# Performance work log

Measured on AMD Instinct MI355X. Metric: run time of the kernel, lower is better.

## Reference

```python
import jax, jax.numpy as jnp
import numpy as np

BN_EPS = 1e-5

def _bn(x, gamma, beta):
    # BatchNorm1d in training mode: batch mean, biased variance
    m = jnp.mean(x, axis=0)
    v = jnp.var(x, axis=0)
    return (x - m) * jax.lax.rsqrt(v + BN_EPS) * gamma + beta

def setup_inputs() -> dict:
    key = jax.random.key(0)
    ks = jax.random.split(key, 12)
    N, E, D, ED = 50000, 600000, 128, 16
    s = lambda k, sh: jax.random.normal(k, sh, dtype=jnp.float32) * 0.05
    return {
        'h': jax.random.normal(ks[0], (N, D), dtype=jnp.float32),
        'edge_index': jax.random.randint(ks[1], (2, E), 0, N, dtype=jnp.int64),
        'edge_attr': jax.random.normal(ks[2], (E, ED), dtype=jnp.float32),
        'ee_w1': s(ks[3], (ED, D)), 'ee_b1': jnp.zeros((D,), jnp.float32),
        'ee_g1': jnp.ones((D,), jnp.float32), 'ee_bb1': jnp.zeros((D,), jnp.float32),
        'ee_w2': s(ks[4], (D, D)), 'ee_b2': jnp.zeros((D,), jnp.float32),
        'mlp_w1': s(ks[5], (D, D)), 'mlp_b1': jnp.zeros((D,), jnp.float32),
        'mlp_g1': jnp.ones((D,), jnp.float32), 'mlp_bb1': jnp.zeros((D,), jnp.float32),
        'mlp_w2': s(ks[6], (D, D)), 'mlp_b2': jnp.zeros((D,), jnp.float32),
        'mlp_g2': jnp.ones((D,), jnp.float32), 'mlp_bb2': jnp.zeros((D,), jnp.float32),
    }

def reference(h, edge_index, edge_attr, ee_w1, ee_b1, ee_g1, ee_bb1, ee_w2, ee_b2,
              mlp_w1, mlp_b1, mlp_g1, mlp_bb1, mlp_w2, mlp_b2, mlp_g2, mlp_bb2):
    N = h.shape[0]
    src, dst = edge_index[0], edge_index[1]
    # edge_encoder: Linear -> BN -> ReLU -> Linear
    e = jax.nn.relu(_bn(edge_attr @ ee_w1 + ee_b1, ee_g1, ee_bb1)) @ ee_w2 + ee_b2  # [E, D]
    # scatter-add edge embeddings to destination nodes
    agg_edge = jax.ops.segment_sum(e, dst, num_segments=N)  # [N, D]
    h = h + agg_edge
    # GINConv (eps=0): mlp(h + sum_{j->i} h_j)
    neigh = jax.ops.segment_sum(h[src], dst, num_segments=N)  # [N, D]
    z = h + neigh
    z = jax.nn.relu(_bn(z @ mlp_w1 + mlp_b1, mlp_g1, mlp_bb1))
    z = jax.nn.relu(_bn(z @ mlp_w2 + mlp_b2, mlp_g2, mlp_bb2))
    return z
```

## Files before the change

kernel.cpp:

```cpp
#include <hip/hip_runtime.h>
#include <hip/hip_bf16.h>

#define DD 128
#define EDIM 16
#define WPB 4
#define PSE 68
#define NCOPY 16

typedef short v8s __attribute__((ext_vector_type(8)));
typedef float v4f __attribute__((ext_vector_type(4)));

__device__ __forceinline__ float ldf(const void* p, int i, int bf){
  return bf ? __bfloat162float(((const __hip_bfloat16*)p)[i])
            : ((const float*)p)[i];
}
__device__ __forceinline__ float bfu_lo(unsigned u){
  unsigned b = (u & 0xffffu) << 16; float f; __builtin_memcpy(&f,&b,4); return f;
}
__device__ __forceinline__ float bfu_hi(unsigned u){
  unsigned b = u & 0xffff0000u; float f; __builtin_memcpy(&f,&b,4); return f;
}
__device__ __forceinline__ unsigned short f2bf(float f){
  unsigned u; __builtin_memcpy(&u,&f,4);
  unsigned r = (u + 0x7fffu + ((u>>16)&1u)) >> 16;
  return (unsigned short)r;
}
__device__ __forceinline__ unsigned packbf(float a, float b){
  return (unsigned)f2bf(a) | ((unsigned)f2bf(b) << 16);
}

__global__ void k_detect(const void* g1, const int* ei, int E, int* flags){
  __shared__ int nz;
  if (threadIdx.x==0) nz = 0;
  __syncthreads();
  long long total = 2LL*E;
  long long stride = (total/1024) & ~1LL;
  if (stride < 2) stride = 2;
  long long idx = (long long)threadIdx.x*stride + 1;
  if (idx < total && ei[idx] != 0) atomicAdd(&nz, 1);
  __syncthreads();
  if (threadIdx.x==0){
    unsigned w = *(const unsigned*)g1;
    flags[0] = (w == 0x3F803F80u) ? 1 : 0;
    flags[1] = (nz == 0) ? 1 : 0;
  }
}

__global__ void k_transB(const void* w0, const void* w1, const void* w2,
                         const void* we1, const int* __restrict__ flags,
                         short* __restrict__ Bt){
  const int bf = flags[0];
  for (int idx = blockIdx.x*blockDim.x + threadIdx.x; idx < 3*16384 + 2048;
       idx += gridDim.x*blockDim.x){
    if (idx < 3*16384){
      int m = idx >> 14, r = idx & 16383;
      int nn = r >> 7, k = r & 127;
      const void* w = (m==0) ? w0 : ((m==1) ? w1 : w2);
      Bt[idx] = (short)f2bf(ldf(w, k*DD + nn, bf));
    } else {
      int r = idx - 3*16384;
      int nn = r >> 4, k = r & 15;
      Bt[idx] = (short)f2bf(ldf(we1, k*DD + nn, bf));
    }
  }
}

__global__ __launch_bounds__(256) void k_attr_moments(
    const void* __restrict__ attr, int E, const int* __restrict__ flags,
    float* __restrict__ Ssum , float* __restrict__ csum )
{
  __shared__ short Ws[4*512];
  __shared__ float sred[4][256];
  __shared__ float credu[4][16];
  const int t = threadIdx.x;
  const int wv = t >> 6, lane = t & 63, l15 = lane & 15, quad = lane >> 4;
  const int bf = flags[0];
  const int el = lane >> 1, half = lane & 1;
  short* W = &Ws[wv*512];

  v4f acc = (v4f){0.f,0.f,0.f,0.f};
  float cs[8];
  #pragma unroll
  for (int j=0;j<8;++j) cs[j]=0.f;

  const int nchunks = (E + 31) >> 5;
  for (int c = blockIdx.x*4 + wv; c < nchunks; c += gridDim.x*4){
    const int e = c*32 + el;
    const bool ok = (e < E);
    float f[8];
    if (bf){
      uint4 u = {0u,0u,0u,0u};
      if (ok) u = reinterpret_cast<const uint4*>(attr)[(size_t)e*2 + half];
      f[0]=bfu_lo(u.x); f[1]=bfu_hi(u.x); f[2]=bfu_lo(u.y); f[3]=bfu_hi(u.y);
      f[4]=bfu_lo(u.z); f[5]=bfu_hi(u.z); f[6]=bfu_lo(u.w); f[7]=bfu_hi(u.w);
    } else {
      float4 v0 = {0,0,0,0}, v1 = {0,0,0,0};
      if (ok){
        const float4* ap = reinterpret_cast<const float4*>(attr) +
                           (size_t)e*4 + half*2;
        v0 = ap[0]; v1 = ap[1];
      }
      f[0]=v0.x; f[1]=v0.y; f[2]=v0.z; f[3]=v0.w;
      f[4]=v1.x; f[5]=v1.y; f[6]=v1.z; f[7]=v1.w;
    }
    #pragma unroll
    for (int j=0;j<8;++j){
      cs[j] += f[j];
      W[(half*8 + j)*32 + el] = (short)f2bf(f[j]);
    }
    v8s a = *reinterpret_cast<const v8s*>(&W[l15*32 + quad*8]);
    acc = __builtin_amdgcn_mfma_f32_16x16x32_bf16(a, a, acc, 0,0,0);
  }

  #pragma unroll
  for (int r=0;r<4;++r) sred[wv][(quad*4 + r)*16 + l15] = acc[r];
  #pragma unroll
  for (int j=0;j<8;++j){
    #pragma unroll
    for (int off=2; off<64; off<<=1) cs[j] += __shfl_xor(cs[j], off, 64);
  }
  if (lane < 2){
    #pragma unroll
    for (int j=0;j<8;++j) credu[wv][lane*8 + j] = cs[j];
  }
  __syncthreads();
  const int cp = blockIdx.x & (NCOPY-1);
  float s = sred[0][t]+sred[1][t]+sred[2][t]+sred[3][t];
  atomicAdd(&Ssum[cp*256 + t], s);
  if (t < 16){
    float s2 = credu[0][t]+credu[1][t]+credu[2][t]+credu[3][t];
    atomicAdd(&csum[cp*16 + t], s2);
  }
}

__global__ void k_edge_bn(const void* __restrict__ w1, const void* __restrict__ g,
                          const void* __restrict__ bb,
                          const float* __restrict__ Ssum, const float* __restrict__ csum,
                          float Einv, const int* __restrict__ flags,
                          float* __restrict__ sc, float* __restrict__ sh){
  __shared__ float fS[256];
  __shared__ float fc[16];
  const int j = threadIdx.x;
  const int bf = flags[0];
  {
    float a0 = 0.f, a1 = 0.f;
    #pragma unroll
    for (int c=0;c<NCOPY;++c){ a0 += Ssum[c*256 + j]; a1 += Ssum[c*256 + 128 + j]; }
    fS[j] = a0; fS[128+j] = a1;
    if (j < 16){
      float a2 = 0.f;
      #pragma unroll
      for (int c=0;c<NCOPY;++c) a2 += csum[c*16 + j];
      fc[j] = a2;
    }
  }
  __syncthreads();
  float w[EDIM];
  #pragma unroll
  for (int p=0;p<EDIM;++p) w[p] = ldf(w1, p*DD + j, bf);
  float mu0 = 0.f;
  #pragma unroll
  for (int p=0;p<EDIM;++p) mu0 += fc[p]*Einv*w[p];
  float s2 = 0.f;
  #pragma unroll
  for (int p=0;p<EDIM;++p){
    float acc = 0.f;
    #pragma unroll
    for (int q=0;q<EDIM;++q) acc += fS[p*16 + q]*w[q];
    s2 += w[p]*acc;
  }
  float var = s2*Einv - mu0*mu0;
  float scv = ldf(g, j, bf) * rsqrtf(var + 1e-5f);
  sc[j] = scv;
  sh[j] = ldf(bb, j, bf) - mu0*scv;
}

__global__ void k_hist(const int* __restrict__ ei, int E,
                       const int* __restrict__ flags, int* __restrict__ deg){
  const int i64 = flags[1];
  const int2* ei2 = (const int2*)ei;
  for (int e = blockIdx.x*blockDim.x + threadIdx.x; e < E;
       e += gridDim.x*blockDim.x){
    int d = i64 ? ei2[E + e].x : ei[E + e];
    atomicAdd(&deg[d], 1);
  }
}

__global__ void k_scan_partial(const int* __restrict__ deg, int n,
                               int* __restrict__ bsum){
  __shared__ int red[256];
  const int t = threadIdx.x;
  const int base = blockIdx.x*1024;
  int s = 0;
  for (int i = t; i < 1024; i += 256){
    int g = base + i;
    s += (g < n) ? deg[g] : 0;
  }
  red[t] = s; __syncthreads();
  for (int off=128; off>0; off>>=1){
    if (t < off) red[t] += red[t+off];
    __syncthreads();
  }
  if (t==0) bsum[blockIdx.x] = red[0];
}

__global__ void k_scan_tops(int* __restrict__ bsum, int nb, int* __restrict__ total){
  __shared__ int buf[256];
  const int t = threadIdx.x;
  int v = (t < nb) ? bsum[t] : 0;
  buf[t] = v; __syncthreads();
  for (int off=1; off<256; off<<=1){
    int x = (t>=off) ? buf[t-off] : 0;
    __syncthreads();
    buf[t] += x; __syncthreads();
  }
  if (t < nb) bsum[t] = buf[t] - v;
  if (t == 255) *total = buf[255];
}

__global__ void k_scan_final(const int* __restrict__ deg, int n, int nwin,
                             const int* __restrict__ bsum, const int* __restrict__ total,
                             int* __restrict__ offsets, int* __restrict__ cursor,
                             int* __restrict__ win2node){
  __shared__ int red[256];
  const int t = threadIdx.x;
  const int base = blockIdx.x*1024 + t*4;
  int v[4]; int s = 0;
  #pragma unroll
  for (int k=0;k<4;++k){
    int g = base + k;
    v[k] = (g < n) ? deg[g] : 0;
    s += v[k];
  }
  red[t] = s; __syncthreads();
  for (int off=1; off<256; off<<=1){
    int x = (t>=off) ? red[t-off] : 0;
    __syncthreads();
    red[t] += x; __syncthreads();
  }
  int ex = bsum[blockIdx.x] + red[t] - s;
  #pragma unroll
  for (int k=0;k<4;++k){
    int g = base + k;
    if (g < n){
      offsets[g] = ex; cursor[g] = ex;
      int end = ex + v[k];
      for (int w = (ex + 63) >> 6; (w << 6) < end; ++w) win2node[w] = g;
    }
    ex += v[k];
  }
  if (blockIdx.x==0 && t==0){
    offsets[n] = *total;
    win2node[nwin] = n - 1;
  }
}

__global__ void k_scatter(const int* __restrict__ ei, int E,
                          const int* __restrict__ flags,
                          int* __restrict__ cursor, int2* __restrict__ se){
  const int i64 = flags[1];
  const int2* ei2 = (const int2*)ei;
  for (int e = blockIdx.x*blockDim.x + threadIdx.x; e < E;
       e += gridDim.x*blockDim.x){
    int d = i64 ? ei2[E + e].x : ei[E + e];
    int s = i64 ? ei2[e].x     : ei[e];
    int pp = atomicAdd(&cursor[d], 1);
    se[pp] = make_int2(s, e);
  }
}

__global__ __launch_bounds__(256) void k_edgeagg(
    const void* __restrict__ attr, const int2* __restrict__ se,
    const short* __restrict__ w1t,
    const float* __restrict__ sc, const float* __restrict__ sh,
    const int* __restrict__ offsets, const int* __restrict__ win2node,
    const int* __restrict__ flags, int n, int E, float* __restrict__ Pagg)
{
  __shared__ __align__(16) float Ps[DD*PSE];
  const int t = threadIdx.x;
  const int wv = t >> 6, lane = t & 63, l15 = lane & 15, quad = lane >> 4;
  const int bf = flags[0];
  const int G0 = blockIdx.x * (64*WPB);
  if (G0 >= E) return;

  const int4 w2nv = *reinterpret_cast<const int4*>(&win2node[blockIdx.x*WPB]);
  const int w2na[4] = {w2nv.x, w2nv.y, w2nv.z, w2nv.w};
  const int w2next = win2node[blockIdx.x*WPB + WPB];

  v8s afrag[WPB];
  #pragma unroll
  for (int w=0; w<WPB; ++w){
    afrag[w] = (v8s){0,0,0,0,0,0,0,0};
    if (quad < 2){
      int slot = G0 + w*64 + wv*16 + l15;
      if (slot < E){
        int e = se[slot].y;
        if (bf){
          afrag[w] = *reinterpret_cast<const v8s*>(
                (const short*)attr + (size_t)e*EDIM + quad*8);
        } else {
          const float4* ap = reinterpret_cast<const float4*>(
                (const float*)attr + (size_t)e*EDIM + quad*8);
          float4 v0 = ap[0], v1 = ap[1];
          v8s av;
          av[0]=(short)f2bf(v0.x); av[1]=(short)f2bf(v0.y);
          av[2]=(short)f2bf(v0.z); av[3]=(short)f2bf(v0.w);
          av[4]=(short)f2bf(v1.x); av[5]=(short)f2bf(v1.y);
          av[6]=(short)f2bf(v1.z); av[7]=(short)f2bf(v1.w);
          afrag[w] = av;
        }
      }
    }
  }

  v8s bfrag[8];
  #pragma unroll
  for (int cg=0;cg<8;++cg){
    bfrag[cg] = (v8s){0,0,0,0,0,0,0,0};
    if (quad < 2)
      bfrag[cg] = *reinterpret_cast<const v8s*>(&w1t[(cg*16+l15)*EDIM + quad*8]);
  }
  const float scA = sc[lane],      shA = sh[lane];
  const float scB = sc[lane + 64], shB = sh[lane + 64];

  #pragma unroll
  for (int w=0; w<WPB; ++w){
    const int B0 = G0 + w*64;
    if (B0 >= E) break;
    const int Bend = (B0 + 64 < E) ? (B0 + 64) : E;

    #pragma unroll
    for (int cg=0;cg<8;++cg){
      v4f acc = (v4f){0.f,0.f,0.f,0.f};
      acc = __builtin_amdgcn_mfma_f32_16x16x32_bf16(bfrag[cg], afrag[w], acc, 0,0,0);
      #pragma unroll
      for (int reg=0;reg<4;++reg)
        Ps[(cg*16 + quad*4 + reg)*PSE + wv*16 + l15] = acc[reg];
    }
    __syncthreads();

    const int i1 = (w < WPB-1) ? w2na[w+1] : w2next;
    int idx = w2na[w] + wv;
    int nb = 0, ne = 0;
    if (idx <= i1){ nb = offsets[idx]; ne = offsets[idx+1]; }
    while (idx <= i1){
      const int idxn = idx + 4;
      int nbn = 0, nen = 0;
      if (idxn <= i1){ nbn = offsets[idxn]; nen = offsets[idxn+1]; }
      int s0 = nb - B0; if (s0 < 0) s0 = 0;
      const int s1 = (ne < Bend ? ne : Bend) - B0;
      if (s1 > s0){
        float sa = 0.f, sb = 0.f;
        const int c1 = (s1 - 1) >> 2;
        for (int cc = s0 >> 2; cc <= c1; ++cc){
          v4f va = *reinterpret_cast<const v4f*>(&Ps[lane*PSE + cc*4]);
          v4f vb = *reinterpret_cast<const v4f*>(&Ps[(lane+64)*PSE + cc*4]);
          #pragma unroll
          for (int k2=0;k2<4;++k2){
            const int r = cc*4 + k2;
            if (r >= s0 && r < s1){
              sa += fmaxf(fmaf(va[k2], scA, shA), 0.f);
              sb += fmaxf(fmaf(vb[k2], scB, shB), 0.f);
            }
          }
        }
        if (nb < B0 || ne > Bend){
          atomicAdd(&Pagg[(size_t)idx*DD + lane], sa);
          atomicAdd(&Pagg[(size_t)idx*DD + lane + 64], sb);
        } else {
          Pagg[(size_t)idx*DD + lane] = sa;
          Pagg[(size_t)idx*DD + lane + 64] = sb;
        }
      }
      nb = nbn; ne = nen; idx = idxn;
    }
    __syncthreads();
  }
}

__global__ __launch_bounds__(256) void k_gather_z(
    const uint4* __restrict__ hnew16, const int* __restrict__ offsets,
    const int2* __restrict__ se, int n, uint4* __restrict__ zH16)
{
  const int wv = threadIdx.x >> 6, lane = threadIdx.x & 63;
  const int g = lane >> 4, c16 = lane & 15;
  for (int i = blockIdx.x*4 + wv; i < n; i += gridDim.x*4){
    const int beg = offsets[i], end = offsets[i+1];
    float a0=0.f,a1=0.f,a2=0.f,a3=0.f,a4=0.f,a5=0.f,a6=0.f,a7=0.f;
    int c0 = beg;
    for (; c0 + 8 <= end; c0 += 8){
      int s1 = se[c0 + g].x;
      int s2 = se[c0 + 4 + g].x;
      uint4 u = hnew16[(size_t)s1*16 + c16];
      uint4 v = hnew16[(size_t)s2*16 + c16];
      a0 += bfu_lo(u.x)+bfu_lo(v.x); a1 += bfu_hi(u.x)+bfu_hi(v.x);
      a2 += bfu_lo(u.y)+bfu_lo(v.y); a3 += bfu_hi(u.y)+bfu_hi(v.y);
      a4 += bfu_lo(u.z)+bfu_lo(v.z); a5 += bfu_hi(u.z)+bfu_hi(v.z);
      a6 += bfu_lo(u.w)+bfu_lo(v.w); a7 += bfu_hi(u.w)+bfu_hi(v.w);
    }
    for (; c0 < end; c0 += 4){
      int r = c0 + g;
      if (r < end){
        uint4 u = hnew16[(size_t)se[r].x*16 + c16];
        a0 += bfu_lo(u.x); a1 += bfu_hi(u.x);
        a2 += bfu_lo(u.y); a3 += bfu_hi(u.y);
        a4 += bfu_lo(u.z); a5 += bfu_hi(u.z);
        a6 += bfu_lo(u.w); a7 += bfu_hi(u.w);
      }
    }
    a0 += __shfl_xor(a0,16,64); a1 += __shfl_xor(a1,16,64);
    a2 += __shfl_xor(a2,16,64); a3 += __shfl_xor(a3,16,64);
    a4 += __shfl_xor(a4,16,64); a5 += __shfl_xor(a5,16,64);
    a6 += __shfl_xor(a6,16,64); a7 += __shfl_xor(a7,16,64);
    a0 += __shfl_xor(a0,32,64); a1 += __shfl_xor(a1,32,64);
    a2 += __shfl_xor(a2,32,64); a3 += __shfl_xor(a3,32,64);
    a4 += __shfl_xor(a4,32,64); a5 += __shfl_xor(a5,32,64);
    a6 += __shfl_xor(a6,32,64); a7 += __shfl_xor(a7,32,64);
    if (lane < 16){
      uint4 m = hnew16[(size_t)i*16 + lane];
      uint4 o;
      o.x = packbf(a0+bfu_lo(m.x), a1+bfu_hi(m.x));
      o.y = packbf(a2+bfu_lo(m.y), a3+bfu_hi(m.y));
      o.z = packbf(a4+bfu_lo(m.z), a5+bfu_hi(m.z));
      o.w = packbf(a6+bfu_lo(m.w), a7+bfu_hi(m.w));
      zH16[(size_t)i*16 + lane] = o;
    }
  }
}

__global__ __launch_bounds__(256) void k_gemm_mfma(
    const short* __restrict__ A, const float* __restrict__ Af32,
    const short* __restrict__ Bt, const void* __restrict__ bias,
    const float* __restrict__ psc, const float* __restrict__ psh,
    const int* __restrict__ deg, const void* __restrict__ H,
    const int* __restrict__ flags, int n,
    __hip_bfloat16* __restrict__ out, float* __restrict__ stats, int mode)
{
  __shared__ float sb[256];
  const int t = threadIdx.x;
  const int bfi = flags[0];
  sb[t] = 0.f;
  __syncthreads();
  const int wv = t >> 6, lane = t & 63, l15 = lane & 15, quad = lane >> 4;
  const int R0 = blockIdx.x*64 + wv*16;

  v8s a[4];
  {
    const int arow = R0 + l15;
    const bool ok = (arow < n);
    #pragma unroll
    for (int ks=0;ks<4;++ks){
      const int k0 = ks*32 + quad*8;
      float f[8];
      if (Af32){
        float4 v0 = {0,0,0,0}, v1 = {0,0,0,0};
        if (ok){
          const float4* ap = reinterpret_cast<const float4*>(
              Af32 + (size_t)arow*DD + k0);
          v0 = ap[0]; v1 = ap[1];
        }
        f[0]=v0.x; f[1]=v0.y; f[2]=v0.z; f[3]=v0.w;
        f[4]=v1.x; f[5]=v1.y; f[6]=v1.z; f[7]=v1.w;
        v8s av;
        #pragma unroll
        for (int j=0;j<8;++j) av[j] = (short)f2bf(f[j]);
        a[ks] = av;
      } else {
        uint4 u = {0u,0u,0u,0u};
        if (ok) u = *reinterpret_cast<const uint4*>(&A[(size_t)arow*DD + k0]);
        if (psc){
          f[0]=bfu_lo(u.x); f[1]=bfu_hi(u.x); f[2]=bfu_lo(u.y); f[3]=bfu_hi(u.y);
          f[4]=bfu_lo(u.z); f[5]=bfu_hi(u.z); f[6]=bfu_lo(u.w); f[7]=bfu_hi(u.w);
          v8s av;
          #pragma unroll
          for (int j=0;j<8;++j)
            av[j] = (short)f2bf(fmaxf(fmaf(f[j], psc[k0+j], psh[k0+j]), 0.f));
          a[ks] = av;
        } else {
          a[ks] = *reinterpret_cast<v8s*>(&u);
        }
      }
    }
  }

  v4f acc[8];
  #pragma unroll
  for (int cg=0;cg<8;++cg) acc[cg] = (v4f){0.f,0.f,0.f,0.f};
  #pragma unroll
  for (int ks=0;ks<4;++ks){
    #pragma unroll
    for (int cg=0;cg<8;++cg){
      v8s b = *reinterpret_cast<const v8s*>(
                &Bt[(cg*16+l15)*DD + ks*32 + quad*8]);
      acc[cg] = __builtin_amdgcn_mfma_f32_16x16x32_bf16(a[ks], b, acc[cg], 0,0,0);
    }
  }

  float bc[8];
  #pragma unroll
  for (int cg=0;cg<8;++cg) bc[cg] = ldf(bias, cg*16 + l15, bfi);
  float ss[8], sq[8];
  #pragma unroll
  for (int cg=0;cg<8;++cg){ ss[cg]=0.f; sq[cg]=0.f; }

  #pragma unroll
  for (int reg=0;reg<4;++reg){
    const int row = R0 + quad*4 + reg;
    if (row < n){
      float degf = (mode==1) ? (float)deg[row] : 0.f;
      #pragma unroll
      for (int cg=0;cg<8;++cg){
        const int col = cg*16 + l15;
        float x = acc[cg][reg];
        if (mode==1) x = fmaf(degf, bc[cg], x) + ldf(H, (size_t)row*DD + col, bfi);
        else         x += bc[cg];
        out[(size_t)row*DD + col] = __float2bfloat16(x);
        ss[cg] += x; sq[cg] += x*x;
      }
    }
  }

  if (stats){
    #pragma unroll
    for (int cg=0;cg<8;++cg){
      float s = ss[cg], q = sq[cg];
      s += __shfl_xor(s, 16, 64); s += __shfl_xor(s, 32, 64);
      q += __shfl_xor(q, 16, 64); q += __shfl_xor(q, 32, 64);
      if (quad == 0){
        atomicAdd(&sb[cg*16 + l15], s);
        atomicAdd(&sb[128 + cg*16 + l15], q);
      }
    }
    __syncthreads();
    atomicAdd(&stats[t], sb[t]);
  }
}

__global__ void k_bn_params(const float* __restrict__ stats, const void* __restrict__ g,
                            const void* __restrict__ bb, const int* __restrict__ flags,
                            float inv_n, float* __restrict__ sc, float* __restrict__ sh){
  const int j = threadIdx.x;
  const int bf = flags[0];
  float mean = stats[j]*inv_n;
  float var  = stats[DD+j]*inv_n - mean*mean;
  float s = ldf(g, j, bf) * rsqrtf(var + 1e-5f);
  sc[j] = s;
  sh[j] = ldf(bb, j, bf) - mean*s;
}

__global__ void k_final(const unsigned* __restrict__ yH,
                        const float* __restrict__ sc, const float* __restrict__ sh,
                        int n, const int* __restrict__ flags, void* __restrict__ out){
  const int bf = flags[0];
  const int nw = n*64;
  for (int i = blockIdx.x*blockDim.x + threadIdx.x; i < nw;
       i += gridDim.x*blockDim.x){
    const int j0 = (i & 63)*2;
    unsigned u = yH[i];
    float v0 = fmaxf(fmaf(bfu_lo(u), sc[j0],   sh[j0]),   0.f);
    float v1 = fmaxf(fmaf(bfu_hi(u), sc[j0+1], sh[j0+1]), 0.f);
    if (bf){
      ((unsigned*)out)[i] = packbf(v0, v1);
    } else {
      *reinterpret_cast<float2*>((float*)out + 2*(size_t)i) = make_float2(v0, v1);
    }
  }
}

extern "C" void kernel_launch(void* const* d_in, const int* in_sizes, int n_in,
                              void* d_out, int out_size, void* d_ws, size_t ws_size,
                              hipStream_t stream)
{
  const void* h       = d_in[0];
  const int*  ei      = (const int*)d_in[1];
  const void* attr    = d_in[2];
  const void* ee_w1   = d_in[3];
  const void* ee_g1   = d_in[5];
  const void* ee_bb1  = d_in[6];
  const void* ee_w2   = d_in[7];
  const void* ee_b2   = d_in[8];
  const void* mlp_w1  = d_in[9];
  const void* mlp_b1  = d_in[10];
  const void* mlp_g1  = d_in[11];
  const void* mlp_bb1 = d_in[12];
  const void* mlp_w2  = d_in[13];
  const void* mlp_b2  = d_in[14];
  const void* mlp_g2  = d_in[15];
  const void* mlp_bb2 = d_in[16];

  const int N = in_sizes[0] / DD;
  const int E = in_sizes[1] / 2;
  const int nb = (N + 1023) / 1024;
  const int e64  = (E + 63) / 64;
  const int e256 = (E + 64*WPB - 1) / (64*WPB);

  char* p = (char*)d_ws;
  auto alloc = [&](size_t bytes)->char*{
    char* r = p;
    p += (bytes + 255) & ~size_t(255);
    return r;
  };
  int* flags = (int*)alloc(8);
  char* zbase = p;
  int*   deg    = (int*)  zbase;
  float* csum   = (float*)(zbase + (size_t)N*4);
  float* Ssum   = (float*)(zbase + (size_t)N*4 + 1024);
  float* stats1 = (float*)(zbase + (size_t)N*4 + 1024 + 16384);
  float* stats2 = (float*)(zbase + (size_t)N*4 + 1024 + 16384 + 1024);
  float* Pagg   = (float*)(zbase + (size_t)N*4 + 1024 + 16384 + 2048);
  size_t zlen   = (size_t)N*4 + 1024 + 16384 + 2048 + (size_t)N*DD*4;
  p += (zlen + 255) & ~size_t(255);
  int*   bsum     = (int*)  alloc(256*4);
  int*   total    = (int*)  alloc(64);
  int*   offsets  = (int*)  alloc((size_t)(N+1)*4);
  int*   cursor   = (int*)  alloc((size_t)N*4);
  int*   win2node = (int*)  alloc((size_t)(e64 + 8)*4);
  int2*  se       = (int2*) alloc((size_t)E*8);
  short* Bt      = (short*)alloc((size_t)(3*DD*DD + DD*EDIM)*2);
  short* w1t     = Bt + 3*DD*DD;
  float* ebn_sc  = (float*)alloc(512);
  float* ebn_sh  = (float*)alloc(512);
  float* sc1     = (float*)alloc(512);
  float* sh1     = (float*)alloc(512);
  float* sc2     = (float*)alloc(512);
  float* sh2     = (float*)alloc(512);
  short* hnewH   = (short*)alloc((size_t)N*DD*2);
  short* zH      = (short*)alloc((size_t)N*DD*2);
  short* y1H     = (short*)alloc((size_t)N*DD*2);
  short* y2H     = (short*)alloc((size_t)N*DD*2);
  (void)ws_size; (void)n_in; (void)out_size;

  const int g64  = (N + 63) / 64;
  const int gseg = (N + 15) / 16;

  hipMemsetAsync(zbase, 0, zlen, stream);
  k_detect<<<1, 1024, 0, stream>>>(ee_g1, ei, E, flags);
  k_transB<<<208, 256, 0, stream>>>(ee_w2, mlp_w1, mlp_w2, ee_w1, flags, Bt);
  k_attr_moments<<<1024, 256, 0, stream>>>(attr, E, flags, Ssum, csum);
  k_edge_bn<<<1, 128, 0, stream>>>(ee_w1, ee_g1, ee_bb1, Ssum, csum,
                                   1.0f/(float)E, flags, ebn_sc, ebn_sh);
  k_hist<<<1024, 256, 0, stream>>>(ei, E, flags, deg);
  k_scan_partial<<<nb, 256, 0, stream>>>(deg, N, bsum);
  k_scan_tops<<<1, 256, 0, stream>>>(bsum, nb, total);
  k_scan_final<<<nb, 256, 0, stream>>>(deg, N, e64, bsum, total, offsets, cursor,
                                       win2node);
  k_scatter<<<1024, 256, 0, stream>>>(ei, E, flags, cursor, se);

  k_edgeagg<<<e256, 256, 0, stream>>>(attr, se, w1t, ebn_sc, ebn_sh,
                                      offsets, win2node, flags, N, E, Pagg);

  k_gemm_mfma<<<g64, 256, 0, stream>>>(nullptr, Pagg, Bt, ee_b2,
                                       nullptr, nullptr, deg, h, flags, N,
                                       (__hip_bfloat16*)hnewH, nullptr, 1);
  k_gather_z<<<gseg, 256, 0, stream>>>((const uint4*)hnewH, offsets, se, N,
                                       (uint4*)zH);
  k_gemm_mfma<<<g64, 256, 0, stream>>>(zH, nullptr, Bt + 16384, mlp_b1,
                                       nullptr, nullptr, nullptr, nullptr,
                                       flags, N, (__hip_bfloat16*)y1H, stats1, 0);
  k_bn_params<<<1, 128, 0, stream>>>(stats1, mlp_g1, mlp_bb1, flags,
                                     1.0f/(float)N, sc1, sh1);
  k_gemm_mfma<<<g64, 256, 0, stream>>>(y1H, nullptr, Bt + 32768, mlp_b2,
                                       sc1, sh1, nullptr, nullptr,
                                       flags, N, (__hip_bfloat16*)y2H, stats2, 0);
  k_bn_params<<<1, 128, 0, stream>>>(stats2, mlp_g2, mlp_bb2, flags,
                                     1.0f/(float)N, sc2, sh2);

  k_final<<<2048, 256, 0, stream>>>((const unsigned*)y2H, sc2, sh2,
                                    N, flags, d_out);
}
```

Before: 444.3 us.

## Merge small prep, scan and BN-parameter kernels to cut launch count

Weight transposition, edge-attribute moments and the degree histogram now run as one block-partitioned launch. The edge BN parameter computation rides along as an extra block of the partial scan, and the top-level scan is folded into each final-scan block. The per-layer BN scale/shift kernels are removed; each GEMM or final block recomputes them from the stats in shared memory. This removes about six small serial launches and their gaps, at the cost of redundant per-block work and heavier shared-memory and register use in the combined kernel.

```diff
diff --git a/kernel.cpp b/kernel.cpp
--- a/kernel.cpp
+++ b/kernel.cpp
@@ -6,6 +6,9 @@
 #define WPB 4
 #define PSE 68
 #define NCOPY 16
+#define PREP_TB 208
+#define PREP_AM 1024
+#define PREP_HI 1024
 
 typedef short v8s __attribute__((ext_vector_type(8)));
 typedef float v4f __attribute__((ext_vector_type(4)));
@@ -46,155 +49,162 @@
   }
 }
 
-__global__ void k_transB(const void* w0, const void* w1, const void* w2,
-                         const void* we1, const int* __restrict__ flags,
-                         short* __restrict__ Bt){
-  const int bf = flags[0];
-  for (int idx = blockIdx.x*blockDim.x + threadIdx.x; idx < 3*16384 + 2048;
-       idx += gridDim.x*blockDim.x){
-    if (idx < 3*16384){
-      int m = idx >> 14, r = idx & 16383;
-      int nn = r >> 7, k = r & 127;
-      const void* w = (m==0) ? w0 : ((m==1) ? w1 : w2);
-      Bt[idx] = (short)f2bf(ldf(w, k*DD + nn, bf));
-    } else {
-      int r = idx - 3*16384;
-      int nn = r >> 4, k = r & 15;
-      Bt[idx] = (short)f2bf(ldf(we1, k*DD + nn, bf));
-    }
-  }
-}
-
-__global__ __launch_bounds__(256) void k_attr_moments(
-    const void* __restrict__ attr, int E, const int* __restrict__ flags,
-    float* __restrict__ Ssum , float* __restrict__ csum )
+__global__ __launch_bounds__(256) void k_prep(
+    const void* w0, const void* w1, const void* w2, const void* we1,
+    const void* __restrict__ attr, const int* __restrict__ ei, int E,
+    const int* __restrict__ flags, short* __restrict__ Bt,
+    float* __restrict__ Ssum, float* __restrict__ csum, int* __restrict__ deg)
 {
-  __shared__ short Ws[4*512];
-  __shared__ float sred[4][256];
-  __shared__ float credu[4][16];
+  const int b = blockIdx.x;
   const int t = threadIdx.x;
-  const int wv = t >> 6, lane = t & 63, l15 = lane & 15, quad = lane >> 4;
-  const int bf = flags[0];
-  const int el = lane >> 1, half = lane & 1;
-  short* W = &Ws[wv*512];
-
-  v4f acc = (v4f){0.f,0.f,0.f,0.f};
-  float cs[8];
-  #pragma unroll
-  for (int j=0;j<8;++j) cs[j]=0.f;
-
-  const int nchunks = (E + 31) >> 5;
-  for (int c = blockIdx.x*4 + wv; c < nchunks; c += gridDim.x*4){
-    const int e = c*32 + el;
-    const bool ok = (e < E);
-    float f[8];
-    if (bf){
-      uint4 u = {0u,0u,0u,0u};
-      if (ok) u = reinterpret_cast<const uint4*>(attr)[(size_t)e*2 + half];
-      f[0]=bfu_lo(u.x); f[1]=bfu_hi(u.x); f[2]=bfu_lo(u.y); f[3]=bfu_hi(u.y);
-      f[4]=bfu_lo(u.z); f[5]=bfu_hi(u.z); f[6]=bfu_lo(u.w); f[7]=bfu_hi(u.w);
-    } else {
-      float4 v0 = {0,0,0,0}, v1 = {0,0,0,0};
-      if (ok){
-        const float4* ap = reinterpret_cast<const float4*>(attr) +
-                           (size_t)e*4 + half*2;
-        v0 = ap[0]; v1 = ap[1];
-      }
-      f[0]=v0.x; f[1]=v0.y; f[2]=v0.z; f[3]=v0.w;
-      f[4]=v1.x; f[5]=v1.y; f[6]=v1.z; f[7]=v1.w;
-    }
+  if (b < PREP_TB){
+    const int bf = flags[0];
+    for (int idx = b*256 + t; idx < 3*16384 + 2048; idx += PREP_TB*256){
+      if (idx < 3*16384){
+        int m = idx >> 14, r = idx & 16383;
+        int nn = r >> 7, k = r & 127;
+        const void* w = (m==0) ? w0 : ((m==1) ? w1 : w2);
+        Bt[idx] = (short)f2bf(ldf(w, k*DD + nn, bf));
+      } else {
+        int r = idx - 3*16384;
+        int nn = r >> 4, k = r & 15;
+        Bt[idx] = (short)f2bf(ldf(we1, k*DD + nn, bf));
+      }
+    }
+    return;
+  }
+  if (b < PREP_TB + PREP_AM){
+    const int rb = b - PREP_TB;
+    __shared__ short Ws[4*512];
+    __shared__ float sred[4][256];
+    __shared__ float credu[4][16];
+    const int wv = t >> 6, lane = t & 63, l15 = lane & 15, quad = lane >> 4;
+    const int bf = flags[0];
+    const int el = lane >> 1, half = lane & 1;
+    short* W = &Ws[wv*512];
+
+    v4f acc = (v4f){0.f,0.f,0.f,0.f};
+    float cs[8];
+    #pragma unroll
+    for (int j=0;j<8;++j) cs[j]=0.f;
+
+    const int nchunks = (E + 31) >> 5;
+    for (int c = rb*4 + wv; c < nchunks; c += PREP_AM*4){
+      const int e = c*32 + el;
+      const bool ok = (e < E);
+      float f[8];
+      if (bf){
+        uint4 u = {0u,0u,0u,0u};
+        if (ok) u = reinterpret_cast<const uint4*>(attr)[(size_t)e*2 + half];
+        f[0]=bfu_lo(u.x); f[1]=bfu_hi(u.x); f[2]=bfu_lo(u.y); f[3]=bfu_hi(u.y);
+        f[4]=bfu_lo(u.z); f[5]=bfu_hi(u.z); f[6]=bfu_lo(u.w); f[7]=bfu_hi(u.w);
+      } else {
+        float4 v0 = {0,0,0,0}, v1 = {0,0,0,0};
+        if (ok){
+          const float4* ap = reinterpret_cast<const float4*>(attr) +
+                             (size_t)e*4 + half*2;
+          v0 = ap[0]; v1 = ap[1];
+        }
+        f[0]=v0.x; f[1]=v0.y; f[2]=v0.z; f[3]=v0.w;
+        f[4]=v1.x; f[5]=v1.y; f[6]=v1.z; f[7]=v1.w;
+      }
+      #pragma unroll
+      for (int j=0;j<8;++j){
+        cs[j] += f[j];
+        W[(half*8 + j)*32 + el] = (short)f2bf(f[j]);
+      }
+      v8s a = *reinterpret_cast<const v8s*>(&W[l15*32 + quad*8]);
+      acc = __builtin_amdgcn_mfma_f32_16x16x32_bf16(a, a, acc, 0,0,0);
+    }
+
+    #pragma unroll
+    for (int r=0;r<4;++r) sred[wv][(quad*4 + r)*16 + l15] = acc[r];
     #pragma unroll
     for (int j=0;j<8;++j){
-      cs[j] += f[j];
-      W[(half*8 + j)*32 + el] = (short)f2bf(f[j]);
-    }
-    v8s a = *reinterpret_cast<const v8s*>(&W[l15*32 + quad*8]);
-    acc = __builtin_amdgcn_mfma_f32_16x16x32_bf16(a, a, acc, 0,0,0);
-  }
-
-  #pragma unroll
-  for (int r=0;r<4;++r) sred[wv][(quad*4 + r)*16 + l15] = acc[r];
-  #pragma unroll
-  for (int j=0;j<8;++j){
-    #pragma unroll
-    for (int off=2; off<64; off<<=1) cs[j] += __shfl_xor(cs[j], off, 64);
-  }
-  if (lane < 2){
-    #pragma unroll
-    for (int j=0;j<8;++j) credu[wv][lane*8 + j] = cs[j];
-  }
-  __syncthreads();
-  const int cp = blockIdx.x & (NCOPY-1);
-  float s = sred[0][t]+sred[1][t]+sred[2][t]+sred[3][t];
-  atomicAdd(&Ssum[cp*256 + t], s);
-  if (t < 16){
-    float s2 = credu[0][t]+credu[1][t]+credu[2][t]+credu[3][t];
-    atomicAdd(&csum[cp*16 + t], s2);
-  }
-}
-
-__global__ void k_edge_bn(const void* __restrict__ w1, const void* __restrict__ g,
-                          const void* __restrict__ bb,
-                          const float* __restrict__ Ssum, const float* __restrict__ csum,
-                          float Einv, const int* __restrict__ flags,
-                          float* __restrict__ sc, float* __restrict__ sh){
-  __shared__ float fS[256];
-  __shared__ float fc[16];
-  const int j = threadIdx.x;
-  const int bf = flags[0];
+      #pragma unroll
+      for (int off=2; off<64; off<<=1) cs[j] += __shfl_xor(cs[j], off, 64);
+    }
+    if (lane < 2){
+      #pragma unroll
+      for (int j=0;j<8;++j) credu[wv][lane*8 + j] = cs[j];
+    }
+    __syncthreads();
+    const int cp = rb & (NCOPY-1);
+    float s = sred[0][t]+sred[1][t]+sred[2][t]+sred[3][t];
+    atomicAdd(&Ssum[cp*256 + t], s);
+    if (t < 16){
+      float s2 = credu[0][t]+credu[1][t]+credu[2][t]+credu[3][t];
+      atomicAdd(&csum[cp*16 + t], s2);
+    }
+    return;
+  }
   {
-    float a0 = 0.f, a1 = 0.f;
-    #pragma unroll
-    for (int c=0;c<NCOPY;++c){ a0 += Ssum[c*256 + j]; a1 += Ssum[c*256 + 128 + j]; }
-    fS[j] = a0; fS[128+j] = a1;
-    if (j < 16){
-      float a2 = 0.f;
-      #pragma unroll
-      for (int c=0;c<NCOPY;++c) a2 += csum[c*16 + j];
-      fc[j] = a2;
-    }
-  }
-  __syncthreads();
-  float w[EDIM];
-  #pragma unroll
-  for (int p=0;p<EDIM;++p) w[p] = ldf(w1, p*DD + j, bf);
-  float mu0 = 0.f;
-  #pragma unroll
-  for (int p=0;p<EDIM;++p) mu0 += fc[p]*Einv*w[p];
-  float s2 = 0.f;
-  #pragma unroll
-  for (int p=0;p<EDIM;++p){
-    float acc = 0.f;
-    #pragma unroll
-    for (int q=0;q<EDIM;++q) acc += fS[p*16 + q]*w[q];
-    s2 += w[p]*acc;
-  }
-  float var = s2*Einv - mu0*mu0;
-  float scv = ldf(g, j, bf) * rsqrtf(var + 1e-5f);
-  sc[j] = scv;
-  sh[j] = ldf(bb, j, bf) - mu0*scv;
-}
-
-__global__ void k_hist(const int* __restrict__ ei, int E,
-                       const int* __restrict__ flags, int* __restrict__ deg){
-  const int i64 = flags[1];
-  const int2* ei2 = (const int2*)ei;
-  for (int e = blockIdx.x*blockDim.x + threadIdx.x; e < E;
-       e += gridDim.x*blockDim.x){
-    int d = i64 ? ei2[E + e].x : ei[E + e];
-    atomicAdd(&deg[d], 1);
-  }
-}
-
-__global__ void k_scan_partial(const int* __restrict__ deg, int n,
-                               int* __restrict__ bsum){
+    const int rb = b - (PREP_TB + PREP_AM);
+    const int i64 = flags[1];
+    const int2* ei2 = (const int2*)ei;
+    for (int e = rb*256 + t; e < E; e += PREP_HI*256){
+      int d = i64 ? ei2[E + e].x : ei[E + e];
+      atomicAdd(&deg[d], 1);
+    }
+  }
+}
+
+__global__ __launch_bounds__(256) void k_scan_pe(
+    const int* __restrict__ deg, int n, int nb,
+    const void* __restrict__ w1, const void* __restrict__ g,
+    const void* __restrict__ bb,
+    const float* __restrict__ Ssum, const float* __restrict__ csum,
+    float Einv, const int* __restrict__ flags,
+    float* __restrict__ sc, float* __restrict__ sh,
+    int* __restrict__ bsum)
+{
+  const int t = threadIdx.x;
+  if ((int)blockIdx.x == nb){
+    __shared__ float fS[256];
+    __shared__ float fc[16];
+    const int bf = flags[0];
+    {
+      float a0 = 0.f;
+      #pragma unroll
+      for (int c=0;c<NCOPY;++c) a0 += Ssum[c*256 + t];
+      fS[t] = a0;
+      if (t < 16){
+        float a2 = 0.f;
+        #pragma unroll
+        for (int c=0;c<NCOPY;++c) a2 += csum[c*16 + t];
+        fc[t] = a2;
+      }
+    }
+    __syncthreads();
+    if (t < 128){
+      const int j = t;
+      float w[EDIM];
+      #pragma unroll
+      for (int p=0;p<EDIM;++p) w[p] = ldf(w1, p*DD + j, bf);
+      float mu0 = 0.f;
+      #pragma unroll
+      for (int p=0;p<EDIM;++p) mu0 += fc[p]*Einv*w[p];
+      float s2 = 0.f;
+      #pragma unroll
+      for (int p=0;p<EDIM;++p){
+        float acc = 0.f;
+        #pragma unroll
+        for (int q=0;q<EDIM;++q) acc += fS[p*16 + q]*w[q];
+        s2 += w[p]*acc;
+      }
+      float var = s2*Einv - mu0*mu0;
+      float scv = ldf(g, j, bf) * rsqrtf(var + 1e-5f);
+      sc[j] = scv;
+      sh[j] = ldf(bb, j, bf) - mu0*scv;
+    }
+    return;
+  }
   __shared__ int red[256];
-  const int t = threadIdx.x;
   const int base = blockIdx.x*1024;
   int s = 0;
   for (int i = t; i < 1024; i += 256){
-    int g = base + i;
-    s += (g < n) ? deg[g] : 0;
+    int gi = base + i;
+    s += (gi < n) ? deg[gi] : 0;
   }
   red[t] = s; __syncthreads();
   for (int off=128; off>0; off>>=1){
@@ -204,33 +214,32 @@
   if (t==0) bsum[blockIdx.x] = red[0];
 }
 
-__global__ void k_scan_tops(int* __restrict__ bsum, int nb, int* __restrict__ total){
-  __shared__ int buf[256];
-  const int t = threadIdx.x;
-  int v = (t < nb) ? bsum[t] : 0;
-  buf[t] = v; __syncthreads();
-  for (int off=1; off<256; off<<=1){
-    int x = (t>=off) ? buf[t-off] : 0;
-    __syncthreads();
-    buf[t] += x; __syncthreads();
-  }
-  if (t < nb) bsum[t] = buf[t] - v;
-  if (t == 255) *total = buf[255];
-}
-
-__global__ void k_scan_final(const int* __restrict__ deg, int n, int nwin,
-                             const int* __restrict__ bsum, const int* __restrict__ total,
+__global__ void k_scan_final(const int* __restrict__ deg, int n, int nwin, int nb,
+                             const int* __restrict__ bsum,
                              int* __restrict__ offsets, int* __restrict__ cursor,
                              int* __restrict__ win2node){
   __shared__ int red[256];
+  __shared__ int pre[2];
   const int t = threadIdx.x;
+  {
+    int v = (t < nb) ? bsum[t] : 0;
+    red[t] = v; __syncthreads();
+    for (int off=1; off<256; off<<=1){
+      int x = (t>=off) ? red[t-off] : 0;
+      __syncthreads();
+      red[t] += x; __syncthreads();
+    }
+    if (t == (int)blockIdx.x) pre[0] = red[t] - v;
+    if (t == 255) pre[1] = red[255];
+    __syncthreads();
+  }
   const int base = blockIdx.x*1024 + t*4;
-  int v[4]; int s = 0;
+  int v4[4]; int s = 0;
   #pragma unroll
   for (int k=0;k<4;++k){
-    int g = base + k;
-    v[k] = (g < n) ? deg[g] : 0;
-    s += v[k];
+    int gi = base + k;
+    v4[k] = (gi < n) ? deg[gi] : 0;
+    s += v4[k];
   }
   red[t] = s; __syncthreads();
   for (int off=1; off<256; off<<=1){
@@ -238,19 +247,19 @@
     __syncthreads();
     red[t] += x; __syncthreads();
   }
-  int ex = bsum[blockIdx.x] + red[t] - s;
+  int ex = pre[0] + red[t] - s;
   #pragma unroll
   for (int k=0;k<4;++k){
-    int g = base + k;
-    if (g < n){
-      offsets[g] = ex; cursor[g] = ex;
-      int end = ex + v[k];
-      for (int w = (ex + 63) >> 6; (w << 6) < end; ++w) win2node[w] = g;
-    }
-    ex += v[k];
+    int gi = base + k;
+    if (gi < n){
+      offsets[gi] = ex; cursor[gi] = ex;
+      int end = ex + v4[k];
+      for (int w = (ex + 63) >> 6; (w << 6) < end; ++w) win2node[w] = gi;
+    }
+    ex += v4[k];
   }
   if (blockIdx.x==0 && t==0){
-    offsets[n] = *total;
+    offsets[n] = pre[1];
     win2node[nwin] = n - 1;
   }
 }
@@ -431,15 +440,24 @@
 __global__ __launch_bounds__(256) void k_gemm_mfma(
     const short* __restrict__ A, const float* __restrict__ Af32,
     const short* __restrict__ Bt, const void* __restrict__ bias,
-    const float* __restrict__ psc, const float* __restrict__ psh,
+    const float* __restrict__ bnstats, const void* __restrict__ bng,
+    const void* __restrict__ bnbb, float bninv,
     const int* __restrict__ deg, const void* __restrict__ H,
     const int* __restrict__ flags, int n,
     __hip_bfloat16* __restrict__ out, float* __restrict__ stats, int mode)
 {
   __shared__ float sb[256];
+  __shared__ float sbn[256];
   const int t = threadIdx.x;
   const int bfi = flags[0];
   sb[t] = 0.f;
+  if (bnstats && t < 128){
+    float mean = bnstats[t]*bninv;
+    float var  = bnstats[DD+t]*bninv - mean*mean;
+    float s = ldf(bng, t, bfi) * rsqrtf(var + 1e-5f);
+    sbn[t] = s;
+    sbn[128+t] = ldf(bnbb, t, bfi) - mean*s;
+  }
   __syncthreads();
   const int wv = t >> 6, lane = t & 63, l15 = lane & 15, quad = lane >> 4;
   const int R0 = blockIdx.x*64 + wv*16;
@@ -468,13 +486,13 @@
       } else {
         uint4 u = {0u,0u,0u,0u};
         if (ok) u = *reinterpret_cast<const uint4*>(&A[(size_t)arow*DD + k0]);
-        if (psc){
+        if (bnstats){
           f[0]=bfu_lo(u.x); f[1]=bfu_hi(u.x); f[2]=bfu_lo(u.y); f[3]=bfu_hi(u.y);
           f[4]=bfu_lo(u.z); f[5]=bfu_hi(u.z); f[6]=bfu_lo(u.w); f[7]=bfu_hi(u.w);
           v8s av;
           #pragma unroll
           for (int j=0;j<8;++j)
-            av[j] = (short)f2bf(fmaxf(fmaf(f[j], psc[k0+j], psh[k0+j]), 0.f));
+            av[j] = (short)f2bf(fmaxf(fmaf(f[j], sbn[k0+j], sbn[128+k0+j]), 0.f));
           a[ks] = av;
         } else {
           a[ks] = *reinterpret_cast<v8s*>(&u);
@@ -536,29 +554,29 @@
   }
 }
 
-__global__ void k_bn_params(const float* __restrict__ stats, const void* __restrict__ g,
-                            const void* __restrict__ bb, const int* __restrict__ flags,
-                            float inv_n, float* __restrict__ sc, float* __restrict__ sh){
-  const int j = threadIdx.x;
+__global__ void k_final(const unsigned* __restrict__ yH,
+                        const float* __restrict__ bnstats,
+                        const void* __restrict__ bng, const void* __restrict__ bnbb,
+                        float bninv, int n, const int* __restrict__ flags,
+                        void* __restrict__ out){
+  __shared__ float sck[128], shk[128];
   const int bf = flags[0];
-  float mean = stats[j]*inv_n;
-  float var  = stats[DD+j]*inv_n - mean*mean;
-  float s = ldf(g, j, bf) * rsqrtf(var + 1e-5f);
-  sc[j] = s;
-  sh[j] = ldf(bb, j, bf) - mean*s;
-}
-
-__global__ void k_final(const unsigned* __restrict__ yH,
-                        const float* __restrict__ sc, const float* __restrict__ sh,
-                        int n, const int* __restrict__ flags, void* __restrict__ out){
-  const int bf = flags[0];
+  const int t = threadIdx.x;
+  if (t < 128){
+    float mean = bnstats[t]*bninv;
+    float var  = bnstats[DD+t]*bninv - mean*mean;
+    float s = ldf(bng, t, bf) * rsqrtf(var + 1e-5f);
+    sck[t] = s;
+    shk[t] = ldf(bnbb, t, bf) - mean*s;
+  }
+  __syncthreads();
   const int nw = n*64;
-  for (int i = blockIdx.x*blockDim.x + threadIdx.x; i < nw;
+  for (int i = blockIdx.x*blockDim.x + t; i < nw;
        i += gridDim.x*blockDim.x){
     const int j0 = (i & 63)*2;
     unsigned u = yH[i];
-    float v0 = fmaxf(fmaf(bfu_lo(u), sc[j0],   sh[j0]),   0.f);
-    float v1 = fmaxf(fmaf(bfu_hi(u), sc[j0+1], sh[j0+1]), 0.f);
+    float v0 = fmaxf(fmaf(bfu_lo(u), sck[j0],   shk[j0]),   0.f);
+    float v1 = fmaxf(fmaf(bfu_hi(u), sck[j0+1], shk[j0+1]), 0.f);
     if (bf){
       ((unsigned*)out)[i] = packbf(v0, v1);
     } else {
@@ -611,7 +629,6 @@
   size_t zlen   = (size_t)N*4 + 1024 + 16384 + 2048 + (size_t)N*DD*4;
   p += (zlen + 255) & ~size_t(255);
   int*   bsum     = (int*)  alloc(256*4);
-  int*   total    = (int*)  alloc(64);
   int*   offsets  = (int*)  alloc((size_t)(N+1)*4);
   int*   cursor   = (int*)  alloc((size_t)N*4);
   int*   win2node = (int*)  alloc((size_t)(e64 + 8)*4);
@@ -620,10 +637,6 @@
   short* w1t     = Bt + 3*DD*DD;
   float* ebn_sc  = (float*)alloc(512);
   float* ebn_sh  = (float*)alloc(512);
-  float* sc1     = (float*)alloc(512);
-  float* sh1     = (float*)alloc(512);
-  float* sc2     = (float*)alloc(512);
-  float* sh2     = (float*)alloc(512);
   short* hnewH   = (short*)alloc((size_t)N*DD*2);
   short* zH      = (short*)alloc((size_t)N*DD*2);
   short* y1H     = (short*)alloc((size_t)N*DD*2);
@@ -635,14 +648,12 @@
 
   hipMemsetAsync(zbase, 0, zlen, stream);
   k_detect<<<1, 1024, 0, stream>>>(ee_g1, ei, E, flags);
-  k_transB<<<208, 256, 0, stream>>>(ee_w2, mlp_w1, mlp_w2, ee_w1, flags, Bt);
-  k_attr_moments<<<1024, 256, 0, stream>>>(attr, E, flags, Ssum, csum);
-  k_edge_bn<<<1, 128, 0, stream>>>(ee_w1, ee_g1, ee_bb1, Ssum, csum,
-                                   1.0f/(float)E, flags, ebn_sc, ebn_sh);
-  k_hist<<<1024, 256, 0, stream>>>(ei, E, flags, deg);
-  k_scan_partial<<<nb, 256, 0, stream>>>(deg, N, bsum);
-  k_scan_tops<<<1, 256, 0, stream>>>(bsum, nb, total);
-  k_scan_final<<<nb, 256, 0, stream>>>(deg, N, e64, bsum, total, offsets, cursor,
+  k_prep<<<PREP_TB + PREP_AM + PREP_HI, 256, 0, stream>>>(
+      ee_w2, mlp_w1, mlp_w2, ee_w1, attr, ei, E, flags, Bt, Ssum, csum, deg);
+  k_scan_pe<<<nb + 1, 256, 0, stream>>>(deg, N, nb, ee_w1, ee_g1, ee_bb1,
+                                        Ssum, csum, 1.0f/(float)E, flags,
+                                        ebn_sc, ebn_sh, bsum);
+  k_scan_final<<<nb, 256, 0, stream>>>(deg, N, e64, nb, bsum, offsets, cursor,
                                        win2node);
   k_scatter<<<1024, 256, 0, stream>>>(ei, E, flags, cursor, se);
 
@@ -650,21 +661,20 @@
                                       offsets, win2node, flags, N, E, Pagg);
 
   k_gemm_mfma<<<g64, 256, 0, stream>>>(nullptr, Pagg, Bt, ee_b2,
-                                       nullptr, nullptr, deg, h, flags, N,
+                                       nullptr, nullptr, nullptr, 0.f,
+                                       deg, h, flags, N,
                                        (__hip_bfloat16*)hnewH, nullptr, 1);
   k_gather_z<<<gseg, 256, 0, stream>>>((const uint4*)hnewH, offsets, se, N,
                                        (uint4*)zH);
   k_gemm_mfma<<<g64, 256, 0, stream>>>(zH, nullptr, Bt + 16384, mlp_b1,
-                                       nullptr, nullptr, nullptr, nullptr,
-                                       flags, N, (__hip_bfloat16*)y1H, stats1, 0);
-  k_bn_params<<<1, 128, 0, stream>>>(stats1, mlp_g1, mlp_bb1, flags,
-                                     1.0f/(float)N, sc1, sh1);
+                                       nullptr, nullptr, nullptr, 0.f,
+                                       nullptr, nullptr, flags, N,
+                                       (__hip_bfloat16*)y1H, stats1, 0);
   k_gemm_mfma<<<g64, 256, 0, stream>>>(y1H, nullptr, Bt + 32768, mlp_b2,
-                                       sc1, sh1, nullptr, nullptr,
-                                       flags, N, (__hip_bfloat16*)y2H, stats2, 0);
-  k_bn_params<<<1, 128, 0, stream>>>(stats2, mlp_g2, mlp_bb2, flags,
-                                     1.0f/(float)N, sc2, sh2);
-
-  k_final<<<2048, 256, 0, stream>>>((const unsigned*)y2H, sc2, sh2,
+                                       stats1, mlp_g1, mlp_bb1, 1.0f/(float)N,
+                                       nullptr, nullptr, flags, N,
+                                       (__hip_bfloat16*)y2H, stats2, 0);
+  k_final<<<2048, 256, 0, stream>>>((const unsigned*)y2H, stats2,
+                                    mlp_g2, mlp_bb2, 1.0f/(float)N,
                                     N, flags, d_out);
 }
```

Result: faster. 400.6 us (-9.8%).
